# Kernel tuning notes

Hardware: AMD Instinct MI355X
Metric: run time of the kernel (lower is better)

Reference implementation:

```python
import jax, jax.numpy as jnp
import numpy as np

CODEBOOK_DIM = 512
CODEBOOK_SIZE = 1024
NUM_GROUPS = 8
D_GROUP = CODEBOOK_DIM // NUM_GROUPS  # 64


def setup_inputs() -> dict:
    key = jax.random.key(0)
    kx, kc = jax.random.split(key)
    x = jax.random.normal(kx, (8, 2048, CODEBOOK_DIM), dtype=jnp.float32)
    # kaiming_uniform_ per group: bound = sqrt(6 / fan_in), fan_in = D_GROUP
    bound = float(np.sqrt(6.0 / D_GROUP))
    codebook = jax.random.uniform(
        kc, (NUM_GROUPS, CODEBOOK_SIZE, D_GROUP),
        minval=-bound, maxval=bound, dtype=jnp.float32)
    return {"x": x, "codebook": codebook}


def reference(x, codebook):
    B, S, D = x.shape
    G, K, d = codebook.shape  # groups, codebook size, per-group dim
    xg = x.reshape(B, S, G, d)
    x_norm = jnp.sum(xg * xg, axis=-1, keepdims=True)          # [B,S,G,1]
    c_norm = jnp.sum(codebook * codebook, axis=-1)             # [G,K]
    cross = jnp.einsum('bsgd,gkd->bsgk', xg, codebook)         # [B,S,G,K]
    dist = x_norm + c_norm[None, None, :, :] - 2.0 * cross
    indices = jnp.argmin(dist, axis=-1)                        # [B,S,G]
    g_idx = jnp.arange(G)[None, None, :]                       # broadcast group ids
    quantized = codebook[g_idx, indices]                       # [B,S,G,d]
    quantized = quantized.reshape(B, S, D)
    # straight-through estimator: x + stop_grad(q - x)
    return x + jax.lax.stop_gradient(quantized - x)
```

## Files before the change

### kernel.cpp

```cpp
#include <hip/hip_runtime.h>


#define NTOK   16384
#define DMODEL 512
#define NGRP   8
#define DG     64
#define NCODE  1024
#define EPS    0.10f

#define STG_ELEM 8192

typedef __attribute__((ext_vector_type(8))) __bf16 bf16x8;
typedef __attribute__((ext_vector_type(4))) float  f32x4;

__device__ __forceinline__ unsigned umin_(unsigned a, unsigned b){ return a<b?a:b; }

__device__ __forceinline__ void top2_(unsigned& best, unsigned& sec, unsigned key)
{
    unsigned bo = best;
    best = umin_(bo, key);
    unsigned ns;
    asm("v_med3_u32 %0, %1, %2, %3" : "=v"(ns) : "v"(bo), "v"(sec), "v"(key));
    sec = ns;
}

__global__ __launch_bounds__(256) void prep_frags(
    const float* __restrict__ cb, __bf16* __restrict__ wb)
{
    int tid  = blockIdx.x * 256 + threadIdx.x;
    int lane = tid & 63;
    int s    = (tid >> 6) & 1;
    int ct   = (tid >> 7) & 63;
    int g    = tid >> 13;
    int code = ct * 16 + (lane & 15);
    int k0   = s * 32 + (lane >> 4) * 8;
    const float* src = cb + ((size_t)g * NCODE + code) * DG + k0;
    bf16x8 v;
    #pragma unroll
    for (int j = 0; j < 8; ++j) v[j] = (__bf16)(-2.0f * src[j]);
    *reinterpret_cast<bf16x8*>(wb + (size_t)tid * 8) = v;
}

__global__ __launch_bounds__(256) void prep_cnorm(
    const float* __restrict__ cb, float* __restrict__ wcn)
{
    int i = blockIdx.x * 256 + threadIdx.x;
    const float4* c4 = reinterpret_cast<const float4*>(cb + (size_t)i * DG);
    float s = 0.0f;
    #pragma unroll
    for (int j = 0; j < 16; ++j) {
        float4 v = c4[j];
        s = fmaf(v.x, v.x, s); s = fmaf(v.y, v.y, s);
        s = fmaf(v.z, v.z, s); s = fmaf(v.w, v.w, s);
    }
    wcn[i] = s;
}

__device__ __forceinline__ float dotc(const float* __restrict__ a,
                                      const float* __restrict__ b)
{
    const float4* a4 = reinterpret_cast<const float4*>(a);
    const float4* b4 = reinterpret_cast<const float4*>(b);
    float s = 0.0f;
    #pragma unroll 4
    for (int j = 0; j < 16; ++j) {
        float4 u = a4[j], v = b4[j];
        s = fmaf(u.x, v.x, s); s = fmaf(u.y, v.y, s);
        s = fmaf(u.z, v.z, s); s = fmaf(u.w, v.w, s);
    }
    return s;
}

__device__ __forceinline__ bf16x8 cvt8(const float* __restrict__ p)
{
    float4 u = *reinterpret_cast<const float4*>(p);
    float4 v = *reinterpret_cast<const float4*>(p + 4);
    bf16x8 r;
    r[0]=(__bf16)u.x; r[1]=(__bf16)u.y; r[2]=(__bf16)u.z; r[3]=(__bf16)u.w;
    r[4]=(__bf16)v.x; r[5]=(__bf16)v.y; r[6]=(__bf16)v.z; r[7]=(__bf16)v.w;
    return r;
}

__global__ __launch_bounds__(256, 2) void vq_mfma_kernel(
    const float*  __restrict__ x,
    const float*  __restrict__ cb,
    const __bf16* __restrict__ wb,
    const float*  __restrict__ wcn,
    float* __restrict__ out)
{
    __shared__ __bf16 bbufA[STG_ELEM];
    __shared__ __bf16 bbufB[STG_ELEM];
    __shared__ float  cn64[NCODE];

    const int tid  = threadIdx.x;
    const int lane = tid & 63;
    const int wv   = tid >> 6;
    const int g    = blockIdx.x & 7;
    const int tile = blockIdx.x >> 3;

    const __bf16* wbg = wb + (size_t)g * (NCODE * DG);
    const int sbase = wv * 2048 + lane * 8;

    bf16x8 r0, r1, r2, r3;

#define LOADSTG(st) do {                                                  \
    const __bf16* sp_ = wbg + (size_t)(st) * STG_ELEM + sbase;            \
    r0 = *reinterpret_cast<const bf16x8*>(sp_);                           \
    r1 = *reinterpret_cast<const bf16x8*>(sp_ + 512);                     \
    r2 = *reinterpret_cast<const bf16x8*>(sp_ + 1024);                    \
    r3 = *reinterpret_cast<const bf16x8*>(sp_ + 1536);                    \
} while (0)

#define WRITESTG(bufp) do {                                               \
    __bf16* dp_ = (bufp) + sbase;                                         \
    *reinterpret_cast<bf16x8*>(dp_)        = r0;                          \
    *reinterpret_cast<bf16x8*>(dp_ + 512)  = r1;                          \
    *reinterpret_cast<bf16x8*>(dp_ + 1024) = r2;                          \
    *reinterpret_cast<bf16x8*>(dp_ + 1536) = r3;                          \
} while (0)

#define COMPUTESTG(bufp, st) do {                                         \
    _Pragma("unroll 2")                                                   \
    for (int ctl_ = 0; ctl_ < 8; ++ctl_) {                                \
        bf16x8 b0_ = *reinterpret_cast<const bf16x8*>((bufp) + ctl_ * 1024 + lane * 8);        \
        bf16x8 b1_ = *reinterpret_cast<const bf16x8*>((bufp) + ctl_ * 1024 + 512 + lane * 8);  \
        const int code_ = (st) * 128 + ctl_ * 16 + row;                   \
        const float cnv_ = cn64[code_];                                   \
        const f32x4 ci_ = {cnv_, cnv_, cnv_, cnv_};                       \
        _Pragma("unroll")                                                 \
        for (int s_ = 0; s_ < 4; ++s_) {                                  \
            f32x4 z_ = __builtin_amdgcn_mfma_f32_16x16x32_bf16(aA[s_], b0_, ci_, 0, 0, 0); \
            f32x4 d_ = __builtin_amdgcn_mfma_f32_16x16x32_bf16(aB[s_], b1_, z_, 0, 0, 0);  \
            _Pragma("unroll")                                             \
            for (int r_ = 0; r_ < 4; ++r_) {                              \
                unsigned key_ = (__float_as_uint(d_[r_]) & 0xFFFFFC00u) | (unsigned)code_; \
                top2_(best[s_][r_], sec[s_][r_], key_);                   \
            }                                                             \
        }                                                                 \
    }                                                                     \
} while (0)

    LOADSTG(0);

    {
        float4 v = reinterpret_cast<const float4*>(wcn + g * NCODE)[tid];
        v.x += 64.0f; v.y += 64.0f; v.z += 64.0f; v.w += 64.0f;
        reinterpret_cast<float4*>(cn64)[tid] = v;
    }

    const int row  = lane & 15;
    const int q    = lane >> 4;
    const int k0   = q * 8;
    const int tok0 = tile * 256 + wv * 64;

    bf16x8 aA[4], aB[4];
    #pragma unroll
    for (int s = 0; s < 4; ++s) {
        const float* xr = x + (size_t)(tok0 + s * 16 + row) * DMODEL + g * DG;
        aA[s] = cvt8(xr + k0);
        aB[s] = cvt8(xr + 32 + k0);
    }

    unsigned best[4][4], sec[4][4];
    #pragma unroll
    for (int s = 0; s < 4; ++s)
        #pragma unroll
        for (int r = 0; r < 4; ++r) { best[s][r] = 0xFFFFFFFFu; sec[s][r] = 0xFFFFFFFFu; }

    WRITESTG(bbufA);
    __syncthreads();

    for (int stp = 0; stp < 4; ++stp) {
        const int stE = stp * 2, stO = stp * 2 + 1;

        LOADSTG(stO);
        COMPUTESTG(bbufA, stE);
        WRITESTG(bbufB);
        __syncthreads();

        if (stp < 3) {
            LOADSTG(stE + 2);
            COMPUTESTG(bbufB, stO);
            WRITESTG(bbufA);
            __syncthreads();
        } else {
            COMPUTESTG(bbufB, stO);
        }
    }

    unsigned mk[4][4];
    #pragma unroll
    for (int s = 0; s < 4; ++s)
        #pragma unroll
        for (int r = 0; r < 4; ++r) mk[s][r] = best[s][r];
    #pragma unroll
    for (int mask = 1; mask < 16; mask <<= 1) {
        #pragma unroll
        for (int s = 0; s < 4; ++s)
            #pragma unroll
            for (int r = 0; r < 4; ++r) {
                unsigned o = (unsigned)__shfl_xor((int)mk[s][r], mask, 64);
                mk[s][r] = umin_(mk[s][r], o);
            }
    }

    const float* cbg  = cb  + (size_t)g * NCODE * DG;
    const float* wcng = wcn + (size_t)g * NCODE;

    #pragma unroll
    for (int s = 0; s < 4; ++s) {
        #pragma unroll
        for (int r = 0; r < 4; ++r) {
            const unsigned m_ = mk[s][r];
            int sel = (int)(m_ & 0x3FFu);
            const float thr = __uint_as_float(m_ & 0xFFFFFC00u) + EPS;
            const float bd  = __uint_as_float(best[s][r] & 0xFFFFFC00u);
            const float sdd = __uint_as_float(sec[s][r]  & 0xFFFFFC00u);
            const bool oth = (bd <= thr && best[s][r] != m_) || (sdd <= thr);
            const unsigned long long bal = __ballot(oth);
            if (((bal >> (q * 16)) & 0xFFFFULL) != 0ULL) {
                const int token = tok0 + s * 16 + q * 4 + r;
                const float* xr = x + (size_t)token * DMODEL + g * DG;
                const float xn = dotc(xr, xr);
                float ed = 1e30f; int ei = 0x7FFFFFFF;
                if (bd <= thr) {
                    const int cc = (int)(best[s][r] & 0x3FFu);
                    float dd = (xn + wcng[cc]) - 2.0f * dotc(xr, cbg + (size_t)cc * DG);
                    if (dd < ed || (dd == ed && cc < ei)) { ed = dd; ei = cc; }
                }
                if (sdd <= thr) {
                    const int cc = (int)(sec[s][r] & 0x3FFu);
                    float dd = (xn + wcng[cc]) - 2.0f * dotc(xr, cbg + (size_t)cc * DG);
                    if (dd < ed || (dd == ed && cc < ei)) { ed = dd; ei = cc; }
                }
                #pragma unroll
                for (int mask = 1; mask < 16; mask <<= 1) {
                    float pd = __shfl_xor(ed, mask, 64);
                    int   pi = __shfl_xor(ei, mask, 64);
                    if (pd < ed || (pd == ed && pi < ei)) { ed = pd; ei = pi; }
                }
                sel = ei;
            }
            const int token = tok0 + s * 16 + q * 4 + r;
            const float4 src = reinterpret_cast<const float4*>(cbg + (size_t)sel * DG)[row];
            reinterpret_cast<float4*>(out + (size_t)token * DMODEL + g * DG)[row] = src;
        }
    }
#undef LOADSTG
#undef WRITESTG
#undef COMPUTESTG
}

__global__ __launch_bounds__(512, 4) void vq_fp32_kernel(
    const float* __restrict__ x,
    const float* __restrict__ cb,
    float* __restrict__ out)
{
    __shared__ float cnl[NGRP][NCODE];
    const int tid  = threadIdx.x;
    const int lane = tid & 63;
    const int wave = tid >> 6;
    const int g    = __builtin_amdgcn_readfirstlane(wave);
    const int token = blockIdx.x * 64 + lane;
    const float* __restrict__ cbg = cb + (size_t)g * NCODE * DG;

    for (int kk = lane; kk < NCODE; kk += 64) {
        const float4* c4 = reinterpret_cast<const float4*>(cbg + kk * DG);
        float s = 0.0f;
        #pragma unroll
        for (int j = 0; j < 16; ++j) {
            float4 v = c4[j];
            s = fmaf(v.x, v.x, s); s = fmaf(v.y, v.y, s);
            s = fmaf(v.z, v.z, s); s = fmaf(v.w, v.w, s);
        }
        cnl[g][kk] = s;
    }
    __syncthreads();

    const float* xr = x + (size_t)token * DMODEL + g * DG;
    float xn = dotc(xr, xr);
    float bestv = 3.4e38f; int bidx = 0;
    for (int k = 0; k < NCODE; ++k) {
        float dist = (xn + cnl[g][k]) - 2.0f * dotc(xr, cbg + (size_t)k * DG);
        if (dist < bestv) { bestv = dist; bidx = k; }
    }
    const float4* q4 = reinterpret_cast<const float4*>(cbg + (size_t)bidx * DG);
    float4* o4 = reinterpret_cast<float4*>(out + (size_t)token * DMODEL + g * DG);
    #pragma unroll
    for (int j = 0; j < 16; ++j) o4[j] = q4[j];
}

extern "C" void kernel_launch(void* const* d_in, const int* in_sizes, int n_in,
                              void* d_out, int out_size, void* d_ws, size_t ws_size,
                              hipStream_t stream) {
    const float* x  = (const float*)d_in[0];
    const float* cb = (const float*)d_in[1];
    float* out = (float*)d_out;

    const size_t wb_bytes = (size_t)NGRP * NCODE * DG * sizeof(__bf16);
    const size_t cn_bytes = (size_t)NGRP * NCODE * sizeof(float);
    if (ws_size < wb_bytes + cn_bytes) {
        vq_fp32_kernel<<<256, 512, 0, stream>>>(x, cb, out);
        return;
    }
    __bf16* wb  = (__bf16*)d_ws;
    float*  wcn = (float*)((char*)d_ws + wb_bytes);

    prep_frags<<<256, 256, 0, stream>>>(cb, wb);
    prep_cnorm<<<32, 256, 0, stream>>>(cb, wcn);
    vq_mfma_kernel<<<512, 256, 0, stream>>>(x, cb, wb, wcn, out);
}
```

Before: 75.37 us.

## Shrink per-wave token tile to 16 and halve codebook stage for higher occupancy

Each wave now handles 16 tokens instead of 64, with a 4x larger grid, a smaller LDS staging buffer (4096 elements, 16 stages) and launch bounds raised to 8 blocks per CU. The aim is to cut register and LDS pressure and raise occupancy and parallelism, hiding latency better. The trade-off is that each codebook fragment loaded from LDS and global memory now feeds only one MFMA pair instead of four, so codebook traffic per token grows fourfold and there are more barriers.

```diff
diff --git a/kernel.cpp b/kernel.cpp
--- a/kernel.cpp
+++ b/kernel.cpp
@@ -8,7 +8,7 @@
 #define NCODE  1024
 #define EPS    0.10f
 
-#define STG_ELEM 8192
+#define STG_ELEM 4096
 
 typedef __attribute__((ext_vector_type(8))) __bf16 bf16x8;
 typedef __attribute__((ext_vector_type(4))) float  f32x4;
@@ -81,7 +81,7 @@
     return r;
 }
 
-__global__ __launch_bounds__(256, 2) void vq_mfma_kernel(
+__global__ __launch_bounds__(256, 8) void vq_mfma_kernel(
     const float*  __restrict__ x,
     const float*  __restrict__ cb,
     const __bf16* __restrict__ wb,
@@ -99,43 +99,37 @@
     const int tile = blockIdx.x >> 3;
 
     const __bf16* wbg = wb + (size_t)g * (NCODE * DG);
-    const int sbase = wv * 2048 + lane * 8;
-
-    bf16x8 r0, r1, r2, r3;
+    const int sbase = tid * 16;
+
+    bf16x8 r0, r1;
 
 #define LOADSTG(st) do {                                                  \
     const __bf16* sp_ = wbg + (size_t)(st) * STG_ELEM + sbase;            \
     r0 = *reinterpret_cast<const bf16x8*>(sp_);                           \
-    r1 = *reinterpret_cast<const bf16x8*>(sp_ + 512);                     \
-    r2 = *reinterpret_cast<const bf16x8*>(sp_ + 1024);                    \
-    r3 = *reinterpret_cast<const bf16x8*>(sp_ + 1536);                    \
+    r1 = *reinterpret_cast<const bf16x8*>(sp_ + 8);                       \
 } while (0)
 
 #define WRITESTG(bufp) do {                                               \
     __bf16* dp_ = (bufp) + sbase;                                         \
-    *reinterpret_cast<bf16x8*>(dp_)        = r0;                          \
-    *reinterpret_cast<bf16x8*>(dp_ + 512)  = r1;                          \
-    *reinterpret_cast<bf16x8*>(dp_ + 1024) = r2;                          \
-    *reinterpret_cast<bf16x8*>(dp_ + 1536) = r3;                          \
+    *reinterpret_cast<bf16x8*>(dp_)     = r0;                             \
+    *reinterpret_cast<bf16x8*>(dp_ + 8) = r1;                             \
 } while (0)
 
 #define COMPUTESTG(bufp, st) do {                                         \
     _Pragma("unroll 2")                                                   \
-    for (int ctl_ = 0; ctl_ < 8; ++ctl_) {                                \
+    for (int ctl_ = 0; ctl_ < 4; ++ctl_) {                                \
         bf16x8 b0_ = *reinterpret_cast<const bf16x8*>((bufp) + ctl_ * 1024 + lane * 8);        \
         bf16x8 b1_ = *reinterpret_cast<const bf16x8*>((bufp) + ctl_ * 1024 + 512 + lane * 8);  \
-        const int code_ = (st) * 128 + ctl_ * 16 + row;                   \
+        const int code_ = (st) * 64 + ctl_ * 16 + row;                    \
         const float cnv_ = cn64[code_];                                   \
         const f32x4 ci_ = {cnv_, cnv_, cnv_, cnv_};                       \
+        f32x4 z_ = __builtin_amdgcn_mfma_f32_16x16x32_bf16(aA, b0_, ci_, 0, 0, 0); \
+        f32x4 d_ = __builtin_amdgcn_mfma_f32_16x16x32_bf16(aB, b1_, z_, 0, 0, 0);  \
+        asm("" : "+v"(d_));                                               \
         _Pragma("unroll")                                                 \
-        for (int s_ = 0; s_ < 4; ++s_) {                                  \
-            f32x4 z_ = __builtin_amdgcn_mfma_f32_16x16x32_bf16(aA[s_], b0_, ci_, 0, 0, 0); \
-            f32x4 d_ = __builtin_amdgcn_mfma_f32_16x16x32_bf16(aB[s_], b1_, z_, 0, 0, 0);  \
-            _Pragma("unroll")                                             \
-            for (int r_ = 0; r_ < 4; ++r_) {                              \
-                unsigned key_ = (__float_as_uint(d_[r_]) & 0xFFFFFC00u) | (unsigned)code_; \
-                top2_(best[s_][r_], sec[s_][r_], key_);                   \
-            }                                                             \
+        for (int r_ = 0; r_ < 4; ++r_) {                                  \
+            unsigned key_ = (__float_as_uint(d_[r_]) & 0xFFFFFC00u) | (unsigned)code_; \
+            top2_(best[r_], sec[r_], key_);                               \
         }                                                                 \
     }                                                                     \
 } while (0)
@@ -151,26 +145,25 @@
     const int row  = lane & 15;
     const int q    = lane >> 4;
     const int k0   = q * 8;
-    const int tok0 = tile * 256 + wv * 64;
-
-    bf16x8 aA[4], aB[4];
-    #pragma unroll
-    for (int s = 0; s < 4; ++s) {
-        const float* xr = x + (size_t)(tok0 + s * 16 + row) * DMODEL + g * DG;
-        aA[s] = cvt8(xr + k0);
-        aB[s] = cvt8(xr + 32 + k0);
-    }
-
-    unsigned best[4][4], sec[4][4];
-    #pragma unroll
-    for (int s = 0; s < 4; ++s)
-        #pragma unroll
-        for (int r = 0; r < 4; ++r) { best[s][r] = 0xFFFFFFFFu; sec[s][r] = 0xFFFFFFFFu; }
+    const int tok0 = tile * 64 + wv * 16;
+
+    bf16x8 aA, aB;
+    {
+        const float* xr = x + (size_t)(tok0 + row) * DMODEL + g * DG;
+        aA = cvt8(xr + k0);
+        aB = cvt8(xr + 32 + k0);
+        asm("" : "+v"(aA));
+        asm("" : "+v"(aB));
+    }
+
+    unsigned best[4], sec[4];
+    #pragma unroll
+    for (int r = 0; r < 4; ++r) { best[r] = 0xFFFFFFFFu; sec[r] = 0xFFFFFFFFu; }
 
     WRITESTG(bbufA);
     __syncthreads();
 
-    for (int stp = 0; stp < 4; ++stp) {
+    for (int stp = 0; stp < 8; ++stp) {
         const int stE = stp * 2, stO = stp * 2 + 1;
 
         LOADSTG(stO);
@@ -178,7 +171,7 @@
         WRITESTG(bbufB);
         __syncthreads();
 
-        if (stp < 3) {
+        if (stp < 7) {
             LOADSTG(stE + 2);
             COMPUTESTG(bbufB, stO);
             WRITESTG(bbufA);
@@ -188,63 +181,56 @@
         }
     }
 
-    unsigned mk[4][4];
-    #pragma unroll
-    for (int s = 0; s < 4; ++s)
-        #pragma unroll
-        for (int r = 0; r < 4; ++r) mk[s][r] = best[s][r];
+    unsigned mk[4];
+    #pragma unroll
+    for (int r = 0; r < 4; ++r) mk[r] = best[r];
     #pragma unroll
     for (int mask = 1; mask < 16; mask <<= 1) {
         #pragma unroll
-        for (int s = 0; s < 4; ++s)
-            #pragma unroll
-            for (int r = 0; r < 4; ++r) {
-                unsigned o = (unsigned)__shfl_xor((int)mk[s][r], mask, 64);
-                mk[s][r] = umin_(mk[s][r], o);
-            }
+        for (int r = 0; r < 4; ++r) {
+            unsigned o = (unsigned)__shfl_xor((int)mk[r], mask, 64);
+            mk[r] = umin_(mk[r], o);
+        }
     }
 
     const float* cbg  = cb  + (size_t)g * NCODE * DG;
     const float* wcng = wcn + (size_t)g * NCODE;
 
     #pragma unroll
-    for (int s = 0; s < 4; ++s) {
-        #pragma unroll
-        for (int r = 0; r < 4; ++r) {
-            const unsigned m_ = mk[s][r];
-            int sel = (int)(m_ & 0x3FFu);
-            const float thr = __uint_as_float(m_ & 0xFFFFFC00u) + EPS;
-            const float bd  = __uint_as_float(best[s][r] & 0xFFFFFC00u);
-            const float sdd = __uint_as_float(sec[s][r]  & 0xFFFFFC00u);
-            const bool oth = (bd <= thr && best[s][r] != m_) || (sdd <= thr);
-            const unsigned long long bal = __ballot(oth);
-            if (((bal >> (q * 16)) & 0xFFFFULL) != 0ULL) {
-                const int token = tok0 + s * 16 + q * 4 + r;
-                const float* xr = x + (size_t)token * DMODEL + g * DG;
-                const float xn = dotc(xr, xr);
-                float ed = 1e30f; int ei = 0x7FFFFFFF;
-                if (bd <= thr) {
-                    const int cc = (int)(best[s][r] & 0x3FFu);
-                    float dd = (xn + wcng[cc]) - 2.0f * dotc(xr, cbg + (size_t)cc * DG);
-                    if (dd < ed || (dd == ed && cc < ei)) { ed = dd; ei = cc; }
-                }
-                if (sdd <= thr) {
-                    const int cc = (int)(sec[s][r] & 0x3FFu);
-                    float dd = (xn + wcng[cc]) - 2.0f * dotc(xr, cbg + (size_t)cc * DG);
-                    if (dd < ed || (dd == ed && cc < ei)) { ed = dd; ei = cc; }
-                }
-                #pragma unroll
-                for (int mask = 1; mask < 16; mask <<= 1) {
-                    float pd = __shfl_xor(ed, mask, 64);
-                    int   pi = __shfl_xor(ei, mask, 64);
-                    if (pd < ed || (pd == ed && pi < ei)) { ed = pd; ei = pi; }
-                }
-                sel = ei;
+    for (int r = 0; r < 4; ++r) {
+        const unsigned m_ = mk[r];
+        int sel = (int)(m_ & 0x3FFu);
+        const float thr = __uint_as_float(m_ & 0xFFFFFC00u) + EPS;
+        const float bd  = __uint_as_float(best[r] & 0xFFFFFC00u);
+        const float sdd = __uint_as_float(sec[r]  & 0xFFFFFC00u);
+        const bool oth = (bd <= thr && best[r] != m_) || (sdd <= thr);
+        const unsigned long long bal = __ballot(oth);
+        if (((bal >> (q * 16)) & 0xFFFFULL) != 0ULL) {
+            const int token = tok0 + q * 4 + r;
+            const float* xr = x + (size_t)token * DMODEL + g * DG;
+            const float xn = dotc(xr, xr);
+            float ed = 1e30f; int ei = 0x7FFFFFFF;
+            if (bd <= thr) {
+                const int cc = (int)(best[r] & 0x3FFu);
+                float dd = (xn + wcng[cc]) - 2.0f * dotc(xr, cbg + (size_t)cc * DG);
+                if (dd < ed || (dd == ed && cc < ei)) { ed = dd; ei = cc; }
             }
-            const int token = tok0 + s * 16 + q * 4 + r;
-            const float4 src = reinterpret_cast<const float4*>(cbg + (size_t)sel * DG)[row];
-            reinterpret_cast<float4*>(out + (size_t)token * DMODEL + g * DG)[row] = src;
-        }
+            if (sdd <= thr) {
+                const int cc = (int)(sec[r] & 0x3FFu);
+                float dd = (xn + wcng[cc]) - 2.0f * dotc(xr, cbg + (size_t)cc * DG);
+                if (dd < ed || (dd == ed && cc < ei)) { ed = dd; ei = cc; }
+            }
+            #pragma unroll
+            for (int mask = 1; mask < 16; mask <<= 1) {
+                float pd = __shfl_xor(ed, mask, 64);
+                int   pi = __shfl_xor(ei, mask, 64);
+                if (pd < ed || (pd == ed && pi < ei)) { ed = pd; ei = pi; }
+            }
+            sel = ei;
+        }
+        const int token = tok0 + q * 4 + r;
+        const float4 src = reinterpret_cast<const float4*>(cbg + (size_t)sel * DG)[row];
+        reinterpret_cast<float4*>(out + (size_t)token * DMODEL + g * DG)[row] = src;
     }
 #undef LOADSTG
 #undef WRITESTG
@@ -308,5 +294,5 @@
 
     prep_frags<<<256, 256, 0, stream>>>(cb, wb);
     prep_cnorm<<<32, 256, 0, stream>>>(cb, wcn);
-    vq_mfma_kernel<<<512, 256, 0, stream>>>(x, cb, wb, wcn, out);
-}
+    vq_mfma_kernel<<<2048, 256, 0, stream>>>(x, cb, wb, wcn, out);
+}
```

Result: faster. 71.15 us (-5.6%).
